# Optimization experiments

Hardware: AMD Instinct MI355X
Metric: run time of the kernel (lower is better)

The kernel has to match this reference:

```python
import jax, jax.numpy as jnp
import numpy as np

N_TYPES = 4
AEV_DIM = 384
HIDDEN = [160, 128, 96]
CELU_ALPHA = 0.1


def _init_params(key):
    dims = [AEV_DIM] + HIDDEN + [1]
    params = {}
    for li in range(len(dims) - 1):
        key, kw = jax.random.split(key)
        scale = 1.0 / np.sqrt(dims[li])
        # stacked over the N_TYPES per-atom-type experts
        params[f"W{li}"] = (jax.random.normal(kw, (N_TYPES, dims[li], dims[li + 1]), dtype=jnp.float32) * scale)
        params[f"b{li}"] = jnp.zeros((N_TYPES, dims[li + 1]), dtype=jnp.float32)
    return params


def setup_inputs() -> dict:
    key = jax.random.key(0)
    k1, k2, k3 = jax.random.split(key, 3)
    B, A = 2048, 64
    species = jax.random.randint(k1, (B, A), 0, N_TYPES, dtype=jnp.int64)
    aev = jax.random.normal(k2, (B, A, AEV_DIM), dtype=jnp.float32)
    inp = {"species": species, "aev": aev}
    inp.update(_init_params(k3))
    return inp


def _mlp(x, t, W0, b0, W1, b1, W2, b2, W3, b3):
    # x: [N, aev_dim] -> [N] per-atom energy for atom type t
    h = jax.nn.celu(x @ W0[t] + b0[t], alpha=CELU_ALPHA)
    h = jax.nn.celu(h @ W1[t] + b1[t], alpha=CELU_ALPHA)
    h = jax.nn.celu(h @ W2[t] + b2[t], alpha=CELU_ALPHA)
    return (h @ W3[t] + b3[t]).reshape(-1)


def reference(species, aev, W0, b0, W1, b1, W2, b2, W3, b3):
    B, A = species.shape
    sp = species.reshape(-1)            # [B*A]
    x = aev.reshape(-1, aev.shape[-1])  # [B*A, aev_dim]
    out = jnp.zeros(sp.shape, dtype=aev.dtype)  # padding_fill = 0
    for t in range(N_TYPES):  # fixed small expert set
        y = _mlp(x, t, W0, b0, W1, b1, W2, b2, W3, b3)
        out = jnp.where(sp == t, y, out)
    energies = out.reshape(B, A).sum(axis=1)  # reduce over atoms
    return species, energies
```

## Files before the change

kernel.cpp:

```cpp
#include <hip/hip_runtime.h>
#include <math.h>


#define NATOMS   131072
#define NMOL     2048
#define AEV      384
#define NTYPES   4
#define MBLK     64
#define PADTOT   (NATOMS + NTYPES * MBLK)
#define NBLK_MLP (PADTOT / MBLK)
#define NBLK_H   512

#define WB_L1 61440
#define WB_L2 81920
#define WB_T  94208

typedef __attribute__((ext_vector_type(8))) short bf16x8;
typedef __attribute__((ext_vector_type(4))) float f32x4;

__device__ __forceinline__ float celu01(float v) {
  return (v > 0.f) ? v : 0.1f * (__expf(v * 10.f) - 1.f);
}
__device__ __forceinline__ unsigned short f2bf(float x) {
  unsigned u = __float_as_uint(x);
  return (unsigned short)((u + 0x7FFFu + ((u >> 16) & 1u)) >> 16);
}
__device__ __forceinline__ float bf2f(unsigned short h) {
  return __uint_as_float(((unsigned)h) << 16);
}


__global__ void k_pre(const int* __restrict__ species, float* __restrict__ out,
                      int* __restrict__ perm, int* __restrict__ hist,
                      const float* __restrict__ W0, const float* __restrict__ W1,
                      const float* __restrict__ W2, unsigned short* __restrict__ WB) {
  const int tid = threadIdx.x, blk = blockIdx.x;
  const int i = blk * 256 + tid;
  perm[i] = -1;
  if (i < NATOMS) out[i] = (float)species[i];
  if (i < NMOL) out[NATOMS + i] = 0.f;

  for (int f = i; f < NTYPES * WB_T; f += PADTOT) {
    const int t = f / WB_T, e0 = f - t * WB_T;
    int base, NT, N;
    const float* W;
    if (e0 < WB_L1)      { base = 0;     NT = 10; N = 160; W = W0 + (size_t)t * AEV * 160; }
    else if (e0 < WB_L2) { base = WB_L1; NT = 8;  N = 128; W = W1 + (size_t)t * 160 * 128; }
    else                 { base = WB_L2; NT = 6;  N = 96;  W = W2 + (size_t)t * 128 * 96; }
    const int e = e0 - base, frag = e >> 9, r = e & 511, lane = r >> 3, j = r & 7;
    const int kt = frag / NT, nt = frag - kt * NT;
    const int k = kt * 32 + ((lane >> 4) << 3) + j, n = nt * 16 + (lane & 15);
    WB[(size_t)t * WB_T + e0] = f2bf(W[k * N + n]);
  }

  if (blk < NBLK_H) {
    const int sp = species[i];
    const int wv = tid >> 6;
    __shared__ int wc[4 * NTYPES];
#pragma unroll
    for (int t = 0; t < NTYPES; ++t) {
      const unsigned long long m = __ballot(sp == t);
      if ((tid & 63) == 0) wc[wv * NTYPES + t] = __popcll(m);
    }
    __syncthreads();
    if (tid < NTYPES)
      hist[tid * NBLK_H + blk] = wc[tid] + wc[4 + tid] + wc[8 + tid] + wc[12 + tid];
  }
}


__global__ void k_scan(const int* __restrict__ hist, int* __restrict__ poff,
                       int* __restrict__ boff) {
  __shared__ int tot[NTYPES], base[NTYPES];
  const int tid = threadIdx.x, wv = tid >> 6, lane = tid & 63;
  int s = 0;
  for (int c = 0; c < 8; ++c) s += hist[wv * NBLK_H + c * 64 + lane];
  for (int off = 32; off; off >>= 1) s += __shfl_down(s, off);
  if (lane == 0) tot[wv] = s;
  __syncthreads();
  if (tid == 0) {
    int acc = 0; poff[0] = 0;
    for (int t = 0; t < NTYPES; ++t) {
      base[t] = acc;
      acc += ((tot[t] + 63) >> 6) << 6;
      poff[t + 1] = acc;
    }
  }
  __syncthreads();
  int carry = base[wv];
  for (int c = 0; c < 8; ++c) {
    const int orig = hist[wv * NBLK_H + c * 64 + lane];
    int v = orig;
    for (int off = 1; off < 64; off <<= 1) {
      const int u = __shfl_up(v, off);
      if (lane >= off) v += u;
    }
    boff[wv * NBLK_H + c * 64 + lane] = carry + v - orig;
    carry += __shfl(v, 63);
  }
}

__global__ void k_scatter(const int* __restrict__ species, const int* __restrict__ boff,
                          int* __restrict__ perm) {
  const int tid = threadIdx.x, blk = blockIdx.x;
  const int i = blk * 256 + tid;
  const int sp = species[i];
  const int wv = tid >> 6;
  __shared__ int wc[4 * NTYPES];
  unsigned long long msel = 0;
#pragma unroll
  for (int t = 0; t < NTYPES; ++t) {
    const unsigned long long m = __ballot(sp == t);
    if ((tid & 63) == 0) wc[wv * NTYPES + t] = __popcll(m);
    if (sp == t) msel = m;
  }
  __syncthreads();
  int woff = 0;
  for (int w = 0; w < wv; ++w) woff += wc[w * NTYPES + sp];
  const int rk = __builtin_amdgcn_mbcnt_hi((unsigned)(msel >> 32),
                 __builtin_amdgcn_mbcnt_lo((unsigned)msel, 0));
  perm[boff[sp * NBLK_H + blk] + woff + rk] = i;
}


__global__ __launch_bounds__(256, 6) void k_mlp(
    const float* __restrict__ aev, const unsigned short* __restrict__ WB,
    const float* __restrict__ b0, const float* __restrict__ b1,
    const float* __restrict__ b2, const float* __restrict__ b3,
    const float* __restrict__ W3,
    const int* __restrict__ poff, const int* __restrict__ perm,
    float* __restrict__ outE)
{
  __shared__ __align__(16) unsigned short ARENA[64 * 168];
  __shared__ float red[256];
  __shared__ int   permS[64];

  const int tid  = threadIdx.x;
  const int lane = tid & 63;
  const int wv   = __builtin_amdgcn_readfirstlane(tid >> 6);
  const int quad = lane >> 4, l15 = lane & 15;
  const int slot0 = blockIdx.x * MBLK;

  if (tid < 64) permS[tid] = perm[slot0 + tid];
  int t_ = (slot0 >= poff[1]) + (slot0 >= poff[2]) + (slot0 >= poff[3]);
  if (t_ > 3) t_ = 3;
  const int t = __builtin_amdgcn_readfirstlane(t_);
  __syncthreads();

  const bf16x8* wb0 = (const bf16x8*)(WB + (size_t)t * WB_T);
  const bf16x8* wb1 = (const bf16x8*)(WB + (size_t)t * WB_T + WB_L1);
  const bf16x8* wb2 = (const bf16x8*)(WB + (size_t)t * WB_T + WB_L2);

  f32x4 acc0[10];
#pragma unroll
  for (int nt = 0; nt < 10; ++nt) {
    const float b = b0[t * 160 + nt * 16 + l15];
    acc0[nt] = (f32x4){b, b, b, b};
  }
  const int sm = tid >> 2, scg = tid & 3;
  const int sai = permS[sm];
  const float4* src = (const float4*)(aev + (size_t)(sai < 0 ? 0 : sai) * AEV);
  for (int s = 0; s < 4; ++s) {
#pragma unroll
    for (int ii = 0; ii < 6; ++ii) {
      const int c4 = scg + ii * 4;
      float4 v = make_float4(0.f, 0.f, 0.f, 0.f);
      if (sai >= 0) v = src[s * 24 + c4];
      ushort4 p = {f2bf(v.x), f2bf(v.y), f2bf(v.z), f2bf(v.w)};
      *(ushort4*)&ARENA[sm * 104 + c4 * 4] = p;
    }
    __syncthreads();
    const int arow = (wv * 16 + l15) * 104 + quad * 8;
#pragma unroll
    for (int ks = 0; ks < 3; ++ks) {
      const bf16x8 a = *(const bf16x8*)&ARENA[arow + ks * 32];
      const int ksg = s * 3 + ks;
#pragma unroll
      for (int nt = 0; nt < 10; ++nt)
        acc0[nt] = __builtin_amdgcn_mfma_f32_16x16x32_bf16(a, wb0[(ksg * 10 + nt) * 64 + lane], acc0[nt], 0, 0, 0);
    }
    __syncthreads();
  }
  {
    const int hrow0 = wv * 16 + quad * 4;
#pragma unroll
    for (int nt = 0; nt < 10; ++nt)
#pragma unroll
      for (int r = 0; r < 4; ++r)
        ARENA[(hrow0 + r) * 168 + nt * 16 + l15] = f2bf(celu01(acc0[nt][r]));
  }
  __syncthreads();

  f32x4 acc1[8];
#pragma unroll
  for (int nt = 0; nt < 8; ++nt) {
    const float b = b1[t * 128 + nt * 16 + l15];
    acc1[nt] = (f32x4){b, b, b, b};
  }
  {
    const int arow = (wv * 16 + l15) * 168 + quad * 8;
#pragma unroll
    for (int ks = 0; ks < 5; ++ks) {
      const bf16x8 a = *(const bf16x8*)&ARENA[arow + ks * 32];
#pragma unroll
      for (int nt = 0; nt < 8; ++nt)
        acc1[nt] = __builtin_amdgcn_mfma_f32_16x16x32_bf16(a, wb1[(ks * 8 + nt) * 64 + lane], acc1[nt], 0, 0, 0);
    }
  }
  __syncthreads();
  {
    const int hrow0 = wv * 16 + quad * 4;
#pragma unroll
    for (int nt = 0; nt < 8; ++nt)
#pragma unroll
      for (int r = 0; r < 4; ++r)
        ARENA[(hrow0 + r) * 136 + nt * 16 + l15] = f2bf(celu01(acc1[nt][r]));
  }
  __syncthreads();

  f32x4 acc2[6];
#pragma unroll
  for (int nt = 0; nt < 6; ++nt) {
    const float b = b2[t * 96 + nt * 16 + l15];
    acc2[nt] = (f32x4){b, b, b, b};
  }
  {
    const int arow = (wv * 16 + l15) * 136 + quad * 8;
#pragma unroll
    for (int ks = 0; ks < 4; ++ks) {
      const bf16x8 a = *(const bf16x8*)&ARENA[arow + ks * 32];
#pragma unroll
      for (int nt = 0; nt < 6; ++nt)
        acc2[nt] = __builtin_amdgcn_mfma_f32_16x16x32_bf16(a, wb2[(ks * 6 + nt) * 64 + lane], acc2[nt], 0, 0, 0);
    }
  }
  __syncthreads();
  {
    const int hrow0 = wv * 16 + quad * 4;
#pragma unroll
    for (int nt = 0; nt < 6; ++nt)
#pragma unroll
      for (int r = 0; r < 4; ++r)
        ARENA[(hrow0 + r) * 104 + nt * 16 + l15] = f2bf(celu01(acc2[nt][r]));
  }
  __syncthreads();

  const float* w3 = W3 + t * 96;
  float part = 0.f;
#pragma unroll
  for (int q = 0; q < 24; ++q) {
    const int c = wv * 24 + q;
    part = fmaf(bf2f(ARENA[lane * 104 + c]), w3[c], part);
  }
  red[wv * 64 + lane] = part;
  __syncthreads();
  if (wv == 0) {
    const float e = red[lane] + red[64 + lane] + red[128 + lane] + red[192 + lane] + b3[t];
    const int ai = permS[lane];
    if (ai >= 0) atomicAdd(&outE[ai >> 6], e);
  }
}


extern "C" void kernel_launch(void* const* d_in, const int* in_sizes, int n_in,
                              void* d_out, int out_size, void* d_ws, size_t ws_size,
                              hipStream_t stream)
{
  const int*   species = (const int*)d_in[0];
  const float* aev     = (const float*)d_in[1];
  const float* W0 = (const float*)d_in[2];
  const float* b0 = (const float*)d_in[3];
  const float* W1 = (const float*)d_in[4];
  const float* b1 = (const float*)d_in[5];
  const float* W2 = (const float*)d_in[6];
  const float* b2 = (const float*)d_in[7];
  const float* W3 = (const float*)d_in[8];
  const float* b3 = (const float*)d_in[9];
  float* out = (float*)d_out;

  int* poff = (int*)d_ws;
  int* hist = poff + 8;
  int* boff = hist + NTYPES * NBLK_H;
  int* perm = boff + NTYPES * NBLK_H;
  unsigned short* WB = (unsigned short*)(perm + PADTOT);

  k_pre    <<<PADTOT / 256, 256, 0, stream>>>(species, out, perm, hist, W0, W1, W2, WB);
  k_scan   <<<1, 256, 0, stream>>>(hist, poff, boff);
  k_scatter<<<NBLK_H, 256, 0, stream>>>(species, boff, perm);
  k_mlp    <<<NBLK_MLP, 256, 0, stream>>>(aev, WB, b0, b1, b2, b3, W3,
                                          poff, perm, out + NATOMS);
}
```

Measured before the change: 384.0 us.

## Give each wave 32 private rows, reuse B fragments, drop block barriers

Raises the MLP block tile from 64 to 128 atoms, so each wave owns 32 rows in a private LDS region. Each weight fragment loaded from global now feeds two MFMAs instead of one, and all __syncthreads calls are removed because waves no longer share LDS. The final layer is reduced in registers with lane shuffles, so the last LDS round trip and the cross-wave reduction go away. In exchange it uses more registers (launch bounds drop to 2 blocks), pads each type to 128 rows, and lowers occupancy.

```diff
diff --git a/kernel.cpp b/kernel.cpp
--- a/kernel.cpp
+++ b/kernel.cpp
@@ -6,7 +6,7 @@
 #define NMOL     2048
 #define AEV      384
 #define NTYPES   4
-#define MBLK     64
+#define MBLK     128
 #define PADTOT   (NATOMS + NTYPES * MBLK)
 #define NBLK_MLP (PADTOT / MBLK)
 #define NBLK_H   512
@@ -17,23 +17,21 @@
 
 typedef __attribute__((ext_vector_type(8))) short bf16x8;
 typedef __attribute__((ext_vector_type(4))) float f32x4;
+typedef unsigned short ushort;
 
 __device__ __forceinline__ float celu01(float v) {
   return (v > 0.f) ? v : 0.1f * (__expf(v * 10.f) - 1.f);
 }
-__device__ __forceinline__ unsigned short f2bf(float x) {
+__device__ __forceinline__ ushort f2bf(float x) {
   unsigned u = __float_as_uint(x);
-  return (unsigned short)((u + 0x7FFFu + ((u >> 16) & 1u)) >> 16);
-}
-__device__ __forceinline__ float bf2f(unsigned short h) {
-  return __uint_as_float(((unsigned)h) << 16);
+  return (ushort)((u + 0x7FFFu + ((u >> 16) & 1u)) >> 16);
 }
 
 
 __global__ void k_pre(const int* __restrict__ species, float* __restrict__ out,
                       int* __restrict__ perm, int* __restrict__ hist,
                       const float* __restrict__ W0, const float* __restrict__ W1,
-                      const float* __restrict__ W2, unsigned short* __restrict__ WB) {
+                      const float* __restrict__ W2, ushort* __restrict__ WB) {
   const int tid = threadIdx.x, blk = blockIdx.x;
   const int i = blk * 256 + tid;
   perm[i] = -1;
@@ -82,7 +80,7 @@
     int acc = 0; poff[0] = 0;
     for (int t = 0; t < NTYPES; ++t) {
       base[t] = acc;
-      acc += ((tot[t] + 63) >> 6) << 6;
+      acc += ((tot[t] + 127) >> 7) << 7;
       poff[t + 1] = acc;
     }
   }
@@ -123,141 +121,156 @@
 }
 
 
-__global__ __launch_bounds__(256, 6) void k_mlp(
-    const float* __restrict__ aev, const unsigned short* __restrict__ WB,
+__global__ __launch_bounds__(256, 2) void k_mlp(
+    const float* __restrict__ aev, const ushort* __restrict__ WB,
     const float* __restrict__ b0, const float* __restrict__ b1,
     const float* __restrict__ b2, const float* __restrict__ b3,
     const float* __restrict__ W3,
     const int* __restrict__ poff, const int* __restrict__ perm,
     float* __restrict__ outE)
 {
-  __shared__ __align__(16) unsigned short ARENA[64 * 168];
-  __shared__ float red[256];
-  __shared__ int   permS[64];
+  __shared__ __align__(16) ushort ARENA[4 * 5376];
 
   const int tid  = threadIdx.x;
   const int lane = tid & 63;
   const int wv   = __builtin_amdgcn_readfirstlane(tid >> 6);
   const int quad = lane >> 4, l15 = lane & 15;
   const int slot0 = blockIdx.x * MBLK;
-
-  if (tid < 64) permS[tid] = perm[slot0 + tid];
+  const int wbase = wv * 5376;
+
   int t_ = (slot0 >= poff[1]) + (slot0 >= poff[2]) + (slot0 >= poff[3]);
   if (t_ > 3) t_ = 3;
   const int t = __builtin_amdgcn_readfirstlane(t_);
-  __syncthreads();
 
   const bf16x8* wb0 = (const bf16x8*)(WB + (size_t)t * WB_T);
   const bf16x8* wb1 = (const bf16x8*)(WB + (size_t)t * WB_T + WB_L1);
   const bf16x8* wb2 = (const bf16x8*)(WB + (size_t)t * WB_T + WB_L2);
 
-  f32x4 acc0[10];
+  const int a  = lane >> 1, ch = lane & 1;
+  const int pa = perm[slot0 + wv * 32 + a];
+  const float4* src = (const float4*)(aev + (size_t)(pa < 0 ? 0 : pa) * AEV);
+
+  f32x4 acc0[10], acc1[10];
 #pragma unroll
   for (int nt = 0; nt < 10; ++nt) {
     const float b = b0[t * 160 + nt * 16 + l15];
     acc0[nt] = (f32x4){b, b, b, b};
-  }
-  const int sm = tid >> 2, scg = tid & 3;
-  const int sai = permS[sm];
-  const float4* src = (const float4*)(aev + (size_t)(sai < 0 ? 0 : sai) * AEV);
-  for (int s = 0; s < 4; ++s) {
-#pragma unroll
-    for (int ii = 0; ii < 6; ++ii) {
-      const int c4 = scg + ii * 4;
-      float4 v = make_float4(0.f, 0.f, 0.f, 0.f);
-      if (sai >= 0) v = src[s * 24 + c4];
-      ushort4 p = {f2bf(v.x), f2bf(v.y), f2bf(v.z), f2bf(v.w)};
-      *(ushort4*)&ARENA[sm * 104 + c4 * 4] = p;
-    }
-    __syncthreads();
-    const int arow = (wv * 16 + l15) * 104 + quad * 8;
-#pragma unroll
-    for (int ks = 0; ks < 3; ++ks) {
-      const bf16x8 a = *(const bf16x8*)&ARENA[arow + ks * 32];
-      const int ksg = s * 3 + ks;
-#pragma unroll
-      for (int nt = 0; nt < 10; ++nt)
-        acc0[nt] = __builtin_amdgcn_mfma_f32_16x16x32_bf16(a, wb0[(ksg * 10 + nt) * 64 + lane], acc0[nt], 0, 0, 0);
-    }
-    __syncthreads();
-  }
-  {
-    const int hrow0 = wv * 16 + quad * 4;
-#pragma unroll
-    for (int nt = 0; nt < 10; ++nt)
-#pragma unroll
-      for (int r = 0; r < 4; ++r)
-        ARENA[(hrow0 + r) * 168 + nt * 16 + l15] = f2bf(celu01(acc0[nt][r]));
-  }
-  __syncthreads();
-
-  f32x4 acc1[8];
+    acc1[nt] = (f32x4){b, b, b, b};
+  }
+#pragma unroll
+  for (int s = 0; s < 6; ++s) {
+    float4 f[8];
+#pragma unroll
+    for (int i = 0; i < 8; ++i) {
+      f[i] = src[s * 16 + ch * 8 + i];
+      if (pa < 0) f[i] = make_float4(0.f, 0.f, 0.f, 0.f);
+    }
+    const int wb = wbase + (s & 1) * 2304 + a * 72 + ch * 32;
+#pragma unroll
+    for (int i = 0; i < 4; ++i) {
+      bf16x8 p = {(short)f2bf(f[2*i].x), (short)f2bf(f[2*i].y),
+                  (short)f2bf(f[2*i].z), (short)f2bf(f[2*i].w),
+                  (short)f2bf(f[2*i+1].x), (short)f2bf(f[2*i+1].y),
+                  (short)f2bf(f[2*i+1].z), (short)f2bf(f[2*i+1].w)};
+      *(bf16x8*)&ARENA[wb + i * 8] = p;
+    }
+#pragma unroll
+    for (int k2 = 0; k2 < 2; ++k2) {
+      const int rb = wbase + (s & 1) * 2304 + k2 * 32 + quad * 8;
+      const bf16x8 a0 = *(const bf16x8*)&ARENA[rb + l15 * 72];
+      const bf16x8 a1 = *(const bf16x8*)&ARENA[rb + (16 + l15) * 72];
+      const int ksg = s * 2 + k2;
+#pragma unroll
+      for (int nt = 0; nt < 10; ++nt) {
+        const bf16x8 bf = wb0[(ksg * 10 + nt) * 64 + lane];
+        acc0[nt] = __builtin_amdgcn_mfma_f32_16x16x32_bf16(a0, bf, acc0[nt], 0, 0, 0);
+        acc1[nt] = __builtin_amdgcn_mfma_f32_16x16x32_bf16(a1, bf, acc1[nt], 0, 0, 0);
+      }
+    }
+  }
+#pragma unroll
+  for (int nt = 0; nt < 10; ++nt)
+#pragma unroll
+    for (int r = 0; r < 4; ++r) {
+      ARENA[wbase + (quad * 4 + r) * 168 + nt * 16 + l15]        = f2bf(celu01(acc0[nt][r]));
+      ARENA[wbase + (16 + quad * 4 + r) * 168 + nt * 16 + l15]   = f2bf(celu01(acc1[nt][r]));
+    }
+
+  f32x4 accB0[8], accB1[8];
 #pragma unroll
   for (int nt = 0; nt < 8; ++nt) {
     const float b = b1[t * 128 + nt * 16 + l15];
-    acc1[nt] = (f32x4){b, b, b, b};
-  }
-  {
-    const int arow = (wv * 16 + l15) * 168 + quad * 8;
-#pragma unroll
-    for (int ks = 0; ks < 5; ++ks) {
-      const bf16x8 a = *(const bf16x8*)&ARENA[arow + ks * 32];
-#pragma unroll
-      for (int nt = 0; nt < 8; ++nt)
-        acc1[nt] = __builtin_amdgcn_mfma_f32_16x16x32_bf16(a, wb1[(ks * 8 + nt) * 64 + lane], acc1[nt], 0, 0, 0);
-    }
-  }
-  __syncthreads();
-  {
-    const int hrow0 = wv * 16 + quad * 4;
-#pragma unroll
-    for (int nt = 0; nt < 8; ++nt)
-#pragma unroll
-      for (int r = 0; r < 4; ++r)
-        ARENA[(hrow0 + r) * 136 + nt * 16 + l15] = f2bf(celu01(acc1[nt][r]));
-  }
-  __syncthreads();
-
-  f32x4 acc2[6];
+    accB0[nt] = (f32x4){b, b, b, b};
+    accB1[nt] = (f32x4){b, b, b, b};
+  }
+#pragma unroll
+  for (int ks = 0; ks < 5; ++ks) {
+    const int rb = wbase + ks * 32 + quad * 8;
+    const bf16x8 a0 = *(const bf16x8*)&ARENA[rb + l15 * 168];
+    const bf16x8 a1 = *(const bf16x8*)&ARENA[rb + (16 + l15) * 168];
+#pragma unroll
+    for (int nt = 0; nt < 8; ++nt) {
+      const bf16x8 bf = wb1[(ks * 8 + nt) * 64 + lane];
+      accB0[nt] = __builtin_amdgcn_mfma_f32_16x16x32_bf16(a0, bf, accB0[nt], 0, 0, 0);
+      accB1[nt] = __builtin_amdgcn_mfma_f32_16x16x32_bf16(a1, bf, accB1[nt], 0, 0, 0);
+    }
+  }
+#pragma unroll
+  for (int nt = 0; nt < 8; ++nt)
+#pragma unroll
+    for (int r = 0; r < 4; ++r) {
+      ARENA[wbase + (quad * 4 + r) * 136 + nt * 16 + l15]      = f2bf(celu01(accB0[nt][r]));
+      ARENA[wbase + (16 + quad * 4 + r) * 136 + nt * 16 + l15] = f2bf(celu01(accB1[nt][r]));
+    }
+
+  f32x4 accC0[6], accC1[6];
 #pragma unroll
   for (int nt = 0; nt < 6; ++nt) {
     const float b = b2[t * 96 + nt * 16 + l15];
-    acc2[nt] = (f32x4){b, b, b, b};
-  }
-  {
-    const int arow = (wv * 16 + l15) * 136 + quad * 8;
-#pragma unroll
-    for (int ks = 0; ks < 4; ++ks) {
-      const bf16x8 a = *(const bf16x8*)&ARENA[arow + ks * 32];
+    accC0[nt] = (f32x4){b, b, b, b};
+    accC1[nt] = (f32x4){b, b, b, b};
+  }
+#pragma unroll
+  for (int ks = 0; ks < 4; ++ks) {
+    const int rb = wbase + ks * 32 + quad * 8;
+    const bf16x8 a0 = *(const bf16x8*)&ARENA[rb + l15 * 136];
+    const bf16x8 a1 = *(const bf16x8*)&ARENA[rb + (16 + l15) * 136];
+#pragma unroll
+    for (int nt = 0; nt < 6; ++nt) {
+      const bf16x8 bf = wb2[(ks * 6 + nt) * 64 + lane];
+      accC0[nt] = __builtin_amdgcn_mfma_f32_16x16x32_bf16(a0, bf, accC0[nt], 0, 0, 0);
+      accC1[nt] = __builtin_amdgcn_mfma_f32_16x16x32_bf16(a1, bf, accC1[nt], 0, 0, 0);
+    }
+  }
+
+  float w3v[6];
+#pragma unroll
+  for (int nt = 0; nt < 6; ++nt) w3v[nt] = W3[t * 96 + nt * 16 + l15];
+  const float b3t = b3[t];
+
+  float pe[2][4];
+#pragma unroll
+  for (int m = 0; m < 2; ++m)
+#pragma unroll
+    for (int r = 0; r < 4; ++r) {
+      float p = 0.f;
 #pragma unroll
       for (int nt = 0; nt < 6; ++nt)
-        acc2[nt] = __builtin_amdgcn_mfma_f32_16x16x32_bf16(a, wb2[(ks * 6 + nt) * 64 + lane], acc2[nt], 0, 0, 0);
-    }
-  }
-  __syncthreads();
-  {
-    const int hrow0 = wv * 16 + quad * 4;
-#pragma unroll
-    for (int nt = 0; nt < 6; ++nt)
-#pragma unroll
-      for (int r = 0; r < 4; ++r)
-        ARENA[(hrow0 + r) * 104 + nt * 16 + l15] = f2bf(celu01(acc2[nt][r]));
-  }
-  __syncthreads();
-
-  const float* w3 = W3 + t * 96;
-  float part = 0.f;
-#pragma unroll
-  for (int q = 0; q < 24; ++q) {
-    const int c = wv * 24 + q;
-    part = fmaf(bf2f(ARENA[lane * 104 + c]), w3[c], part);
-  }
-  red[wv * 64 + lane] = part;
-  __syncthreads();
-  if (wv == 0) {
-    const float e = red[lane] + red[64 + lane] + red[128 + lane] + red[192 + lane] + b3[t];
-    const int ai = permS[lane];
-    if (ai >= 0) atomicAdd(&outE[ai >> 6], e);
+        p = fmaf(celu01(m ? accC1[nt][r] : accC0[nt][r]), w3v[nt], p);
+      p += __shfl_xor(p, 1);
+      p += __shfl_xor(p, 2);
+      p += __shfl_xor(p, 4);
+      p += __shfl_xor(p, 8);
+      pe[m][r] = p;
+    }
+  if (l15 == 0) {
+#pragma unroll
+    for (int m = 0; m < 2; ++m)
+#pragma unroll
+      for (int r = 0; r < 4; ++r) {
+        const int ai = perm[slot0 + wv * 32 + m * 16 + quad * 4 + r];
+        if (ai >= 0) atomicAdd(&outE[ai >> 6], pe[m][r] + b3t);
+      }
   }
 }
 
@@ -282,7 +295,7 @@
   int* hist = poff + 8;
   int* boff = hist + NTYPES * NBLK_H;
   int* perm = boff + NTYPES * NBLK_H;
-  unsigned short* WB = (unsigned short*)(perm + PADTOT);
+  ushort* WB = (ushort*)(perm + PADTOT);
 
   k_pre    <<<PADTOT / 256, 256, 0, stream>>>(species, out, perm, hist, W0, W1, W2, WB);
   k_scan   <<<1, 256, 0, stream>>>(hist, poff, boff);
```

Result: slower. 398.7 us (+3.8%).
